# Optimization experiments

Measured on AMD Instinct MI355X. Metric: run time of the kernel, lower is better.

## Reference

```python
import jax, jax.numpy as jnp
import numpy as np

DIM = 768
NUM_HEAD = 12
DIM_HEAD = DIM // NUM_HEAD
SCALE = DIM_HEAD ** -0.5
B, N = 4, 1024


def setup_inputs() -> dict:
    key = jax.random.key(0)
    ks = jax.random.split(key, 6)
    return {
        "x": jax.random.normal(ks[0], (B, N, DIM), jnp.float32),
        "q_weight": jax.random.normal(ks[1], (DIM, DIM), jnp.float32) * 0.02,
        "k_weight": jax.random.normal(ks[2], (DIM, DIM), jnp.float32) * 0.02,
        "v_weight": jax.random.normal(ks[3], (DIM, DIM), jnp.float32) * 0.02,
        "q_bias": jnp.zeros((DIM,), jnp.float32),
        "k_bias": jnp.zeros((DIM,), jnp.float32),
        "v_bias": jnp.zeros((DIM,), jnp.float32),
        "proj_weight": jax.random.normal(ks[4], (DIM, DIM), jnp.float32) * 0.02,
        "proj_bias": jax.random.normal(ks[5], (DIM,), jnp.float32) * 0.02,
    }


def reference(x, q_weight, k_weight, v_weight, q_bias, k_bias, v_bias,
              proj_weight, proj_bias):
    B_, N_, C = x.shape
    shortcut = x
    # pre-norm: torch .std() is unbiased (ddof=1)
    mean = jnp.mean(x, axis=-1, keepdims=True)
    std = jnp.std(x, axis=-1, keepdims=True, ddof=1)
    xn = (x - mean) / std
    # F.linear: x @ W.T + b
    q = xn @ q_weight.T + q_bias
    k = xn @ k_weight.T + k_bias
    v = xn @ v_weight.T + v_bias
    # b n (h d) -> b h n d
    q = q.reshape(B_, N_, NUM_HEAD, DIM_HEAD).transpose(0, 2, 1, 3)
    k = k.reshape(B_, N_, NUM_HEAD, DIM_HEAD).transpose(0, 2, 1, 3)
    v = v.reshape(B_, N_, NUM_HEAD, DIM_HEAD).transpose(0, 2, 1, 3)
    attn = jnp.einsum('bhqd,bhkd->bhqk', q, k * SCALE)
    attn = jax.nn.softmax(attn, axis=-1)
    out = jnp.einsum('bhqk,bhkd->bhqd', attn, v)
    out = out.transpose(0, 2, 1, 3).reshape(B_, N_, C)
    out = out @ proj_weight.T + proj_bias
    return out + shortcut
```

## Files before the change

### kernel.cpp

```cpp
#include <hip/hip_runtime.h>

typedef unsigned short ushort_t;
typedef unsigned int uint_t;
typedef __attribute__((ext_vector_type(8))) unsigned short ushort8;
typedef __attribute__((ext_vector_type(2))) unsigned int uint2v;
typedef __attribute__((ext_vector_type(8))) __bf16 bf16x8;
typedef __attribute__((ext_vector_type(4))) float floatx4;

#define DIM 768
#define NHEAD 12
#define DHEAD 64
#define SEQ 1024
#define BATCH 4
#define TOKENS (BATCH * SEQ)
#define WELEM (DIM * DIM)
#define SCALE_LOG2E 0.18033688011112042f

static __device__ __forceinline__ uint_t fbits(float f) {
  union { float f; uint_t u; } c; c.f = f; return c.u;
}
static __device__ __forceinline__ ushort_t f2bf(float f) {
  return (ushort_t)((fbits(f) + 0x8000u) >> 16);
}
static __device__ __forceinline__ uint_t pack_bf2(float lo, float hi) {
  const uint_t a = fbits(lo) + 0x8000u, b = fbits(hi) + 0x8000u;
#if __has_builtin(__builtin_amdgcn_perm)
  return __builtin_amdgcn_perm(b, a, 0x07060302u);
#else
  return (a >> 16) | (b & 0xFFFF0000u);
#endif
}
static __device__ __forceinline__ float fexp2(float x) {
#if __has_builtin(__builtin_amdgcn_exp2f)
  return __builtin_amdgcn_exp2f(x);
#else
  return exp2f(x);
#endif
}
static __device__ __forceinline__ floatx4 mfma16(ushort8 a, ushort8 b, floatx4 c) {
  return __builtin_amdgcn_mfma_f32_16x16x32_bf16(
      __builtin_bit_cast(bf16x8, a), __builtin_bit_cast(bf16x8, b), c, 0, 0, 0);
}
static __device__ __forceinline__ void gload_lds16(const ushort_t* g,
                                                   ushort_t* l) {
  __builtin_amdgcn_global_load_lds(
      (const __attribute__((address_space(1))) void*)g,
      (__attribute__((address_space(3))) void*)l, 16, 0, 0);
}

__global__ __launch_bounds__(256) void prep_kernel(
    const float* __restrict__ qw, const float* __restrict__ kw,
    const float* __restrict__ vw, const float* __restrict__ pw,
    const float* __restrict__ x, ushort_t* __restrict__ wbf,
    ushort_t* __restrict__ xn) {
  const int bid = blockIdx.x;
  if (bid < 2304) {
    const int mat = bid / 576, inner = bid % 576;
    const float* s = (mat == 0) ? qw : (mat == 1) ? kw : (mat == 2) ? vw : pw;
    ushort_t* d = wbf + (size_t)mat * WELEM;
    const int i = (inner * 256 + threadIdx.x) * 4;
    const float4 f = *(const float4*)&s[i];
    uint2v o;
    o[0] = pack_bf2(f.x, f.y);
    o[1] = pack_bf2(f.z, f.w);
    *(uint2v*)&d[i] = o;
  } else {
    const int wave = threadIdx.x >> 6, lane = threadIdx.x & 63;
    const int row = (bid - 2304) * 4 + wave;
    const float4* xr = (const float4*)(x + (size_t)row * DIM);
    float4 v[3];
    float s = 0.f, s2 = 0.f;
#pragma unroll
    for (int j = 0; j < 3; ++j) {
      v[j] = xr[j * 64 + lane];
      s += v[j].x + v[j].y + v[j].z + v[j].w;
      s2 += v[j].x * v[j].x + v[j].y * v[j].y + v[j].z * v[j].z +
            v[j].w * v[j].w;
    }
#pragma unroll
    for (int off = 1; off < 64; off <<= 1) {
      s += __shfl_xor(s, off);
      s2 += __shfl_xor(s2, off);
    }
    const float mean = s * (1.f / 768.f);
    const float var = (s2 - 768.f * mean * mean) * (1.f / 767.f);
    const float rstd = rsqrtf(var);
    ushort_t* xo = xn + (size_t)row * DIM;
#pragma unroll
    for (int j = 0; j < 3; ++j) {
      uint2v o;
      o[0] = pack_bf2((v[j].x - mean) * rstd, (v[j].y - mean) * rstd);
      o[1] = pack_bf2((v[j].z - mean) * rstd, (v[j].w - mean) * rstd);
      *(uint2v*)&xo[(j * 64 + lane) * 4] = o;
    }
  }
}

#define BK 64
#define NKIT (DIM / BK)
__global__ __launch_bounds__(256) void qkv_kernel(
    const ushort_t* __restrict__ xn, const ushort_t* __restrict__ wbf,
    const float* __restrict__ qb, const float* __restrict__ kb,
    const float* __restrict__ vb,
    ushort_t* __restrict__ qh, ushort_t* __restrict__ kh,
    ushort_t* __restrict__ vt) {
  __shared__ ushort_t As[2][128 * BK];
  __shared__ ushort_t Bs[2][128 * BK];
  const int tid = threadIdx.x;
  const int wave = tid >> 6, lane = tid & 63, quad = lane >> 4, l15 = lane & 15;
  const int m0 = blockIdx.x * 128;
  const int mat = blockIdx.y / 6, nb = blockIdx.y % 6;
  const int n0 = nb * 128;
  const ushort_t* W = wbf + (size_t)mat * WELEM;
  const int chan_off = (wave >> 1) * 64, tok_off = (wave & 1) * 64;
  const int srow8 = lane >> 3;
  const int schunk = (lane & 7) ^ srow8;
  const int l7 = l15 & 7;

  floatx4 acc[4][4];
#pragma unroll
  for (int i = 0; i < 4; ++i)
#pragma unroll
    for (int j = 0; j < 4; ++j) acc[i][j] = (floatx4){0.f, 0.f, 0.f, 0.f};

  auto stage = [&](int k0, int bf) {
#pragma unroll
    for (int i = 0; i < 4; ++i) {
      const int c = wave * 4 + i;
      const int row = c * 8 + srow8;
      gload_lds16(&xn[(size_t)(m0 + row) * DIM + k0 + schunk * 8],
                  &As[bf][c * 512]);
      gload_lds16(&W[(size_t)(n0 + row) * DIM + k0 + schunk * 8],
                  &Bs[bf][c * 512]);
    }
  };

  stage(0, 0);
  for (int it = 0; it < NKIT; ++it) {
    const int cur = it & 1;
    __syncthreads();
    if (it + 1 < NKIT) stage((it + 1) * BK, cur ^ 1);
    ushort8 af[4][2], bfr[4][2];
#pragma unroll
    for (int i = 0; i < 4; ++i)
#pragma unroll
      for (int k2 = 0; k2 < 2; ++k2) {
        const int ch = ((k2 * 4 + quad) ^ l7) * 8;
        bfr[i][k2] = *(const ushort8*)&Bs[cur][(chan_off + i * 16 + l15) * BK + ch];
        af[i][k2] = *(const ushort8*)&As[cur][(tok_off + i * 16 + l15) * BK + ch];
      }
#pragma unroll
    for (int k2 = 0; k2 < 2; ++k2)
#pragma unroll
      for (int i = 0; i < 4; ++i)
#pragma unroll
        for (int j = 0; j < 4; ++j)
          acc[i][j] = mfma16(bfr[i][k2], af[j][k2], acc[i][j]);
  }

  if (mat != 2) {
    const float* bias = (mat == 0) ? qb : kb;
    ushort_t* dst = (mat == 0) ? qh : kh;
    const float os = (mat == 0) ? SCALE_LOG2E : 1.0f;
    const int hh = (n0 + chan_off) >> 6;
#pragma unroll
    for (int i = 0; i < 4; ++i) {
      const int ch0 = n0 + chan_off + i * 16 + quad * 4;
      const float4 bv = *(const float4*)&bias[ch0];
      const int d0 = i * 16 + quad * 4;
#pragma unroll
      for (int j = 0; j < 4; ++j) {
        const int tok = m0 + tok_off + j * 16 + l15;
        const int bb = tok >> 10, nn = tok & 1023;
        uint2v pk;
        pk[0] = pack_bf2((acc[i][j][0] + bv.x) * os, (acc[i][j][1] + bv.y) * os);
        pk[1] = pack_bf2((acc[i][j][2] + bv.z) * os, (acc[i][j][3] + bv.w) * os);
        *(uint2v*)&dst[(size_t)((bb * NHEAD + hh) * SEQ + nn) * DHEAD + d0] = pk;
      }
    }
  } else {
    const int tokg = m0 + tok_off;
    const int bb = tokg >> 10, gg = tokg & 1023;
#pragma unroll
    for (int i = 0; i < 4; ++i) {
      const int ch0 = n0 + chan_off + i * 16 + quad * 4;
      const float4 bv = *(const float4*)&vb[ch0];
      const float bvf[4] = {bv.x, bv.y, bv.z, bv.w};
      const int hh = ch0 >> 6, d0 = ch0 & 63;
#pragma unroll
      for (int r = 0; r < 4; ++r) {
        const size_t base = (size_t)((bb * NHEAD + hh) * DHEAD + d0 + r) * SEQ;
        uint2v pk;
        pk[0] = pack_bf2(acc[i][0][r] + bvf[r], acc[i][1][r] + bvf[r]);
        pk[1] = pack_bf2(acc[i][2][r] + bvf[r], acc[i][3][r] + bvf[r]);
        *(uint2v*)&vt[base + gg + l15 * 4] = pk;
      }
    }
  }
}

#define PSTR 68
__global__ __launch_bounds__(256) void attn_kernel(
    const ushort_t* __restrict__ qh, const ushort_t* __restrict__ kh,
    const ushort_t* __restrict__ vt, ushort_t* __restrict__ ao) {
  __shared__ ushort_t kv[2][2][4096];
  __shared__ ushort_t Ps[4][16 * PSTR];
  float* cb = (float*)&kv[0][0][0];
  const int tid = threadIdx.x;
  const int wave = tid >> 6, lane = tid & 63, quad = lane >> 4, l15 = lane & 15;
  const int l7 = l15 & 7;
  const int grp = wave >> 1, wsub = wave & 1;
  const int bid = blockIdx.x;
  const int idx = bid >> 3;
  const int hb = (bid & 7) * 6 + idx % 6;
  const int qb = idx / 6;
  const int h = hb % NHEAD, b = hb / NHEAD;
  const int basekv = ((b * NHEAD + h) * SEQ) * DHEAD;
  const int basevt = ((b * NHEAD + h) * DHEAD) * SEQ;
  const int q0 = qb * 64 + wsub * 32;
  const int kbase = grp * 512;

  ushort8 qf[2][2];
#pragma unroll
  for (int w = 0; w < 2; ++w) {
    const ushort_t* Qr = qh + basekv + (q0 + w * 16 + l15) * DHEAD;
    qf[w][0] = *(const ushort8*)&Qr[quad * 8];
    qf[w][1] = *(const ushort8*)&Qr[32 + quad * 8];
  }
  ushort8 ones;
#pragma unroll
  for (int i = 0; i < 8; ++i) ones[i] = 0x3F80;

  floatx4 o[2][4];
#pragma unroll
  for (int w = 0; w < 2; ++w)
#pragma unroll
    for (int t = 0; t < 4; ++t) o[w][t] = (floatx4){0.f, 0.f, 0.f, 0.f};
  floatx4 acc_l[2] = {(floatx4){0.f, 0.f, 0.f, 0.f},
                      (floatx4){0.f, 0.f, 0.f, 0.f}};

  const int srow8 = lane >> 3, schunk = (lane & 7) ^ srow8;

  for (int kt = 0; kt < 512; kt += 64) {
#pragma unroll
    for (int i = 0; i < 4; ++i) {
      const int c = wsub * 4 + i;
      gload_lds16(&kh[basekv + (kbase + kt + c * 8 + srow8) * DHEAD + schunk * 8],
                  &kv[grp][0][c * 512]);
      gload_lds16(&vt[basevt + (c * 8 + srow8) * SEQ + kbase + kt + schunk * 8],
                  &kv[grp][1][c * 512]);
    }
    __syncthreads();

    floatx4 sacc[2][4];
#pragma unroll
    for (int w = 0; w < 2; ++w)
#pragma unroll
      for (int s = 0; s < 4; ++s) sacc[w][s] = (floatx4){0.f, 0.f, 0.f, 0.f};
#pragma unroll
    for (int s = 0; s < 4; ++s) {
#pragma unroll
      for (int hh = 0; hh < 2; ++hh) {
        const ushort8 kf = *(const ushort8*)&kv[grp][0][(s * 16 + l15) * 64 +
                                                        (((hh * 4 + quad) ^ l7) * 8)];
#pragma unroll
        for (int w = 0; w < 2; ++w)
          sacc[w][s] = mfma16(qf[w][hh], kf, sacc[w][s]);
      }
    }

#pragma unroll
    for (int w = 0; w < 2; ++w) {
#pragma unroll
      for (int r = 0; r < 4; ++r) {
        uint2v pk;
        pk[0] = pack_bf2(fexp2(sacc[w][0][r]), fexp2(sacc[w][1][r]));
        pk[1] = pack_bf2(fexp2(sacc[w][2][r]), fexp2(sacc[w][3][r]));
        *(uint2v*)&Ps[wave][(quad * 4 + r) * PSTR + l15 * 4] = pk;
      }
    }

#pragma unroll
    for (int hh = 0; hh < 2; ++hh) {
      ushort8 pf[2];
#pragma unroll
      for (int w = 0; w < 2; ++w) {
        pf[w] = *(const ushort8*)&Ps[wave][l15 * PSTR + hh * 32 + quad * 8];
        acc_l[w] = mfma16(pf[w], ones, acc_l[w]);
      }
#pragma unroll
      for (int t = 0; t < 4; ++t) {
        const ushort8 vf = *(const ushort8*)&kv[grp][1][(t * 16 + l15) * 64 +
                                                        (((hh * 4 + quad) ^ l7) * 8)];
#pragma unroll
        for (int w = 0; w < 2; ++w) o[w][t] = mfma16(pf[w], vf, o[w][t]);
      }
    }
    __syncthreads();
  }

  const int cb0 = wsub * (32 * 66);
  if (grp == 1) {
#pragma unroll
    for (int w = 0; w < 2; ++w) {
#pragma unroll
      for (int t = 0; t < 4; ++t)
#pragma unroll
        for (int r = 0; r < 4; ++r)
          cb[cb0 + (w * 16 + quad * 4 + r) * 66 + t * 16 + l15] = o[w][t][r];
      if (l15 == 0)
#pragma unroll
        for (int r = 0; r < 4; ++r)
          cb[cb0 + (w * 16 + quad * 4 + r) * 66 + 64] = acc_l[w][r];
    }
  }
  __syncthreads();
  if (grp == 0) {
#pragma unroll
    for (int w = 0; w < 2; ++w) {
#pragma unroll
      for (int r = 0; r < 4; ++r) {
        const int row = w * 16 + quad * 4 + r;
        const float l = acc_l[w][r] + cb[cb0 + row * 66 + 64];
        const float rl = 1.f / l;
        const int token = b * SEQ + q0 + row;
#pragma unroll
        for (int t = 0; t < 4; ++t) {
          const float val = o[w][t][r] + cb[cb0 + row * 66 + t * 16 + l15];
          ao[(size_t)token * DIM + h * DHEAD + t * 16 + l15] = f2bf(val * rl);
        }
      }
    }
  }
}

__global__ __launch_bounds__(256) void proj_kernel(
    const ushort_t* __restrict__ ao, const ushort_t* __restrict__ pwb,
    const float* __restrict__ pb, const float* __restrict__ x,
    float* __restrict__ out) {
  __shared__ ushort_t As[2][64 * BK];
  __shared__ ushort_t Bs[2][128 * BK];
  const int tid = threadIdx.x;
  const int wave = tid >> 6, lane = tid & 63, quad = lane >> 4, l15 = lane & 15;
  const int m0 = blockIdx.x * 64;
  const int n0 = blockIdx.y * 128;
  const int chan_off = (wave >> 1) * 64, tok_off = (wave & 1) * 32;
  const int srow8 = lane >> 3;
  const int schunk = (lane & 7) ^ srow8;
  const int l7 = l15 & 7;

  floatx4 acc[4][2];
#pragma unroll
  for (int i = 0; i < 4; ++i)
#pragma unroll
    for (int j = 0; j < 2; ++j) acc[i][j] = (floatx4){0.f, 0.f, 0.f, 0.f};

  auto stage = [&](int k0, int bf) {
#pragma unroll
    for (int i = 0; i < 2; ++i) {
      const int c = wave * 2 + i;
      const int row = c * 8 + srow8;
      gload_lds16(&ao[(size_t)(m0 + row) * DIM + k0 + schunk * 8],
                  &As[bf][c * 512]);
    }
#pragma unroll
    for (int i = 0; i < 4; ++i) {
      const int c = wave * 4 + i;
      const int row = c * 8 + srow8;
      gload_lds16(&pwb[(size_t)(n0 + row) * DIM + k0 + schunk * 8],
                  &Bs[bf][c * 512]);
    }
  };

  stage(0, 0);
  for (int it = 0; it < NKIT; ++it) {
    const int cur = it & 1;
    __syncthreads();
    if (it + 1 < NKIT) stage((it + 1) * BK, cur ^ 1);
    ushort8 af[2][2], bfr[4][2];
#pragma unroll
    for (int k2 = 0; k2 < 2; ++k2) {
      const int ch = ((k2 * 4 + quad) ^ l7) * 8;
#pragma unroll
      for (int j = 0; j < 2; ++j)
        af[j][k2] = *(const ushort8*)&As[cur][(tok_off + j * 16 + l15) * BK + ch];
#pragma unroll
      for (int i = 0; i < 4; ++i)
        bfr[i][k2] = *(const ushort8*)&Bs[cur][(chan_off + i * 16 + l15) * BK + ch];
    }
#pragma unroll
    for (int k2 = 0; k2 < 2; ++k2)
#pragma unroll
      for (int i = 0; i < 4; ++i)
#pragma unroll
        for (int j = 0; j < 2; ++j)
          acc[i][j] = mfma16(bfr[i][k2], af[j][k2], acc[i][j]);
  }

#pragma unroll
  for (int i = 0; i < 4; ++i) {
    const int ch0 = n0 + chan_off + i * 16 + quad * 4;
    const float4 bv = *(const float4*)&pb[ch0];
#pragma unroll
    for (int j = 0; j < 2; ++j) {
      const int tok = m0 + tok_off + j * 16 + l15;
      const float4 res = *(const float4*)&x[(size_t)tok * DIM + ch0];
      float4 ov;
      ov.x = acc[i][j][0] + bv.x + res.x;
      ov.y = acc[i][j][1] + bv.y + res.y;
      ov.z = acc[i][j][2] + bv.z + res.z;
      ov.w = acc[i][j][3] + bv.w + res.w;
      *(float4*)&out[(size_t)tok * DIM + ch0] = ov;
    }
  }
}

extern "C" void kernel_launch(void* const* d_in, const int* in_sizes, int n_in,
                              void* d_out, int out_size, void* d_ws,
                              size_t ws_size, hipStream_t stream) {
  const float* x  = (const float*)d_in[0];
  const float* qw = (const float*)d_in[1];
  const float* kw = (const float*)d_in[2];
  const float* vw = (const float*)d_in[3];
  const float* qb = (const float*)d_in[4];
  const float* kb = (const float*)d_in[5];
  const float* vb = (const float*)d_in[6];
  const float* pw = (const float*)d_in[7];
  const float* pb = (const float*)d_in[8];
  float* out = (float*)d_out;

  ushort_t* ws = (ushort_t*)d_ws;
  const size_t NTOK = (size_t)TOKENS * DIM;
  ushort_t* xn  = ws;
  ushort_t* qh  = ws + NTOK;
  ushort_t* kh  = ws + 2 * NTOK;
  ushort_t* vt  = ws + 3 * NTOK;
  ushort_t* wbf = ws + 4 * NTOK;
  ushort_t* ao  = xn;

  prep_kernel<<<2304 + TOKENS / 4, 256, 0, stream>>>(qw, kw, vw, pw, x, wbf, xn);
  qkv_kernel<<<dim3(32, 18), 256, 0, stream>>>(xn, wbf, qb, kb, vb, qh, kh, vt);
  attn_kernel<<<768, 256, 0, stream>>>(qh, kh, vt, ao);
  proj_kernel<<<dim3(64, 6), 256, 0, stream>>>(ao, wbf + 3 * (size_t)WELEM, pb,
                                               x, out);
}
```

Before: 152.9 us.

## Halve QKV token tile and double-buffer K/V tiles in attention

The QKV GEMM drops its token tile from 128 to 64 rows per block, which doubles the grid to 1152 blocks for better occupancy and load balance, and the V-transpose epilogue is adjusted to match. The attention kernel switches from single-buffered 64-key tiles with two barriers per iteration to double-buffered 32-key tiles, prefetching the next tile while computing the current one, with one barrier per iteration. The V tile uses a new swizzle for its 32-wide rows, and the probability scratch is split per query sub-tile. The trade-off is less reuse per block in the GEMM and more loop iterations and barriers of smaller MFMA work in attention.

```diff
diff --git a/kernel.cpp b/kernel.cpp
--- a/kernel.cpp
+++ b/kernel.cpp
@@ -104,33 +104,36 @@
     const float* __restrict__ vb,
     ushort_t* __restrict__ qh, ushort_t* __restrict__ kh,
     ushort_t* __restrict__ vt) {
-  __shared__ ushort_t As[2][128 * BK];
+  __shared__ ushort_t As[2][64 * BK];
   __shared__ ushort_t Bs[2][128 * BK];
   const int tid = threadIdx.x;
   const int wave = tid >> 6, lane = tid & 63, quad = lane >> 4, l15 = lane & 15;
-  const int m0 = blockIdx.x * 128;
+  const int m0 = blockIdx.x * 64;
   const int mat = blockIdx.y / 6, nb = blockIdx.y % 6;
   const int n0 = nb * 128;
   const ushort_t* W = wbf + (size_t)mat * WELEM;
-  const int chan_off = (wave >> 1) * 64, tok_off = (wave & 1) * 64;
+  const int chan_off = (wave >> 1) * 64, tok_off = (wave & 1) * 32;
   const int srow8 = lane >> 3;
   const int schunk = (lane & 7) ^ srow8;
   const int l7 = l15 & 7;
 
-  floatx4 acc[4][4];
+  floatx4 acc[4][2];
 #pragma unroll
   for (int i = 0; i < 4; ++i)
 #pragma unroll
-    for (int j = 0; j < 4; ++j) acc[i][j] = (floatx4){0.f, 0.f, 0.f, 0.f};
+    for (int j = 0; j < 2; ++j) acc[i][j] = (floatx4){0.f, 0.f, 0.f, 0.f};
 
   auto stage = [&](int k0, int bf) {
+#pragma unroll
+    for (int i = 0; i < 2; ++i) {
+      const int c = wave * 2 + i;
+      gload_lds16(&xn[(size_t)(m0 + c * 8 + srow8) * DIM + k0 + schunk * 8],
+                  &As[bf][c * 512]);
+    }
 #pragma unroll
     for (int i = 0; i < 4; ++i) {
       const int c = wave * 4 + i;
-      const int row = c * 8 + srow8;
-      gload_lds16(&xn[(size_t)(m0 + row) * DIM + k0 + schunk * 8],
-                  &As[bf][c * 512]);
-      gload_lds16(&W[(size_t)(n0 + row) * DIM + k0 + schunk * 8],
+      gload_lds16(&W[(size_t)(n0 + c * 8 + srow8) * DIM + k0 + schunk * 8],
                   &Bs[bf][c * 512]);
     }
   };
@@ -140,21 +143,23 @@
     const int cur = it & 1;
     __syncthreads();
     if (it + 1 < NKIT) stage((it + 1) * BK, cur ^ 1);
-    ushort8 af[4][2], bfr[4][2];
-#pragma unroll
-    for (int i = 0; i < 4; ++i)
-#pragma unroll
-      for (int k2 = 0; k2 < 2; ++k2) {
-        const int ch = ((k2 * 4 + quad) ^ l7) * 8;
+    ushort8 af[2][2], bfr[4][2];
+#pragma unroll
+    for (int k2 = 0; k2 < 2; ++k2) {
+      const int ch = ((k2 * 4 + quad) ^ l7) * 8;
+#pragma unroll
+      for (int j = 0; j < 2; ++j)
+        af[j][k2] = *(const ushort8*)&As[cur][(tok_off + j * 16 + l15) * BK + ch];
+#pragma unroll
+      for (int i = 0; i < 4; ++i)
         bfr[i][k2] = *(const ushort8*)&Bs[cur][(chan_off + i * 16 + l15) * BK + ch];
-        af[i][k2] = *(const ushort8*)&As[cur][(tok_off + i * 16 + l15) * BK + ch];
-      }
+    }
 #pragma unroll
     for (int k2 = 0; k2 < 2; ++k2)
 #pragma unroll
       for (int i = 0; i < 4; ++i)
 #pragma unroll
-        for (int j = 0; j < 4; ++j)
+        for (int j = 0; j < 2; ++j)
           acc[i][j] = mfma16(bfr[i][k2], af[j][k2], acc[i][j]);
   }
 
@@ -169,7 +174,7 @@
       const float4 bv = *(const float4*)&bias[ch0];
       const int d0 = i * 16 + quad * 4;
 #pragma unroll
-      for (int j = 0; j < 4; ++j) {
+      for (int j = 0; j < 2; ++j) {
         const int tok = m0 + tok_off + j * 16 + l15;
         const int bb = tok >> 10, nn = tok & 1023;
         uint2v pk;
@@ -190,22 +195,20 @@
 #pragma unroll
       for (int r = 0; r < 4; ++r) {
         const size_t base = (size_t)((bb * NHEAD + hh) * DHEAD + d0 + r) * SEQ;
-        uint2v pk;
-        pk[0] = pack_bf2(acc[i][0][r] + bvf[r], acc[i][1][r] + bvf[r]);
-        pk[1] = pack_bf2(acc[i][2][r] + bvf[r], acc[i][3][r] + bvf[r]);
-        *(uint2v*)&vt[base + gg + l15 * 4] = pk;
+        *(uint_t*)&vt[base + gg + l15 * 2] =
+            pack_bf2(acc[i][0][r] + bvf[r], acc[i][1][r] + bvf[r]);
       }
     }
   }
 }
 
-#define PSTR 68
+#define PSTR2 34
 __global__ __launch_bounds__(256) void attn_kernel(
     const ushort_t* __restrict__ qh, const ushort_t* __restrict__ kh,
     const ushort_t* __restrict__ vt, ushort_t* __restrict__ ao) {
-  __shared__ ushort_t kv[2][2][4096];
-  __shared__ ushort_t Ps[4][16 * PSTR];
-  float* cb = (float*)&kv[0][0][0];
+  __shared__ ushort_t kv[2][2][2][2048];
+  __shared__ ushort_t Ps[4][2][16 * PSTR2];
+  float* cb = (float*)&kv[0][0][0][0];
   const int tid = threadIdx.x;
   const int wave = tid >> 6, lane = tid & 63, quad = lane >> 4, l15 = lane & 15;
   const int l7 = l15 & 7;
@@ -239,30 +242,40 @@
   floatx4 acc_l[2] = {(floatx4){0.f, 0.f, 0.f, 0.f},
                       (floatx4){0.f, 0.f, 0.f, 0.f}};
 
-  const int srow8 = lane >> 3, schunk = (lane & 7) ^ srow8;
-
-  for (int kt = 0; kt < 512; kt += 64) {
-#pragma unroll
-    for (int i = 0; i < 4; ++i) {
-      const int c = wsub * 4 + i;
-      gload_lds16(&kh[basekv + (kbase + kt + c * 8 + srow8) * DHEAD + schunk * 8],
-                  &kv[grp][0][c * 512]);
-      gload_lds16(&vt[basevt + (c * 8 + srow8) * SEQ + kbase + kt + schunk * 8],
-                  &kv[grp][1][c * 512]);
-    }
+  const int ksrow = lane >> 3, kschunk = (lane & 7) ^ ksrow;
+  const int vdrow = lane >> 2;
+  const int vchunk = (lane & 3) ^ ((vdrow >> 1) & 3);
+
+  auto stage = [&](int kt, int bf) {
+#pragma unroll
+    for (int i = 0; i < 2; ++i) {
+      const int c = wsub * 2 + i;
+      gload_lds16(&kh[basekv + (kt + c * 8 + ksrow) * DHEAD + kschunk * 8],
+                  &kv[grp][bf][0][c * 512]);
+      gload_lds16(&vt[basevt + (c * 16 + vdrow) * SEQ + kt + vchunk * 8],
+                  &kv[grp][bf][1][c * 512]);
+    }
+  };
+
+  stage(kbase, 0);
+  for (int it = 0; it < 16; ++it) {
+    const int cur = it & 1;
     __syncthreads();
-
-    floatx4 sacc[2][4];
+    if (it + 1 < 16) stage(kbase + (it + 1) * 32, cur ^ 1);
+    const ushort_t* K = &kv[grp][cur][0][0];
+    const ushort_t* V = &kv[grp][cur][1][0];
+
+    floatx4 sacc[2][2];
 #pragma unroll
     for (int w = 0; w < 2; ++w)
 #pragma unroll
-      for (int s = 0; s < 4; ++s) sacc[w][s] = (floatx4){0.f, 0.f, 0.f, 0.f};
-#pragma unroll
-    for (int s = 0; s < 4; ++s) {
+      for (int s = 0; s < 2; ++s) sacc[w][s] = (floatx4){0.f, 0.f, 0.f, 0.f};
+#pragma unroll
+    for (int s = 0; s < 2; ++s) {
 #pragma unroll
       for (int hh = 0; hh < 2; ++hh) {
-        const ushort8 kf = *(const ushort8*)&kv[grp][0][(s * 16 + l15) * 64 +
-                                                        (((hh * 4 + quad) ^ l7) * 8)];
+        const ushort8 kf = *(const ushort8*)&K[(s * 16 + l15) * 64 +
+                                               (((hh * 4 + quad) ^ l7) * 8)];
 #pragma unroll
         for (int w = 0; w < 2; ++w)
           sacc[w][s] = mfma16(qf[w][hh], kf, sacc[w][s]);
@@ -270,34 +283,27 @@
     }
 
 #pragma unroll
+    for (int w = 0; w < 2; ++w)
+#pragma unroll
+      for (int r = 0; r < 4; ++r)
+        *(uint_t*)&Ps[wave][w][(quad * 4 + r) * PSTR2 + l15 * 2] =
+            pack_bf2(fexp2(sacc[w][0][r]), fexp2(sacc[w][1][r]));
+
+    ushort8 pf[2];
+#pragma unroll
     for (int w = 0; w < 2; ++w) {
-#pragma unroll
-      for (int r = 0; r < 4; ++r) {
-        uint2v pk;
-        pk[0] = pack_bf2(fexp2(sacc[w][0][r]), fexp2(sacc[w][1][r]));
-        pk[1] = pack_bf2(fexp2(sacc[w][2][r]), fexp2(sacc[w][3][r]));
-        *(uint2v*)&Ps[wave][(quad * 4 + r) * PSTR + l15 * 4] = pk;
-      }
-    }
-
-#pragma unroll
-    for (int hh = 0; hh < 2; ++hh) {
-      ushort8 pf[2];
-#pragma unroll
-      for (int w = 0; w < 2; ++w) {
-        pf[w] = *(const ushort8*)&Ps[wave][l15 * PSTR + hh * 32 + quad * 8];
-        acc_l[w] = mfma16(pf[w], ones, acc_l[w]);
-      }
-#pragma unroll
-      for (int t = 0; t < 4; ++t) {
-        const ushort8 vf = *(const ushort8*)&kv[grp][1][(t * 16 + l15) * 64 +
-                                                        (((hh * 4 + quad) ^ l7) * 8)];
-#pragma unroll
-        for (int w = 0; w < 2; ++w) o[w][t] = mfma16(pf[w], vf, o[w][t]);
-      }
-    }
-    __syncthreads();
-  }
+      pf[w] = *(const ushort8*)&Ps[wave][w][l15 * PSTR2 + quad * 8];
+      acc_l[w] = mfma16(pf[w], ones, acc_l[w]);
+    }
+#pragma unroll
+    for (int t = 0; t < 4; ++t) {
+      const ushort8 vf = *(const ushort8*)&V[(t * 16 + l15) * 32 +
+                                             ((quad ^ ((l15 >> 1) & 3)) * 8)];
+#pragma unroll
+      for (int w = 0; w < 2; ++w) o[w][t] = mfma16(pf[w], vf, o[w][t]);
+    }
+  }
+  __syncthreads();
 
   const int cb0 = wsub * (32 * 66);
   if (grp == 1) {
@@ -359,15 +365,13 @@
 #pragma unroll
     for (int i = 0; i < 2; ++i) {
       const int c = wave * 2 + i;
-      const int row = c * 8 + srow8;
-      gload_lds16(&ao[(size_t)(m0 + row) * DIM + k0 + schunk * 8],
+      gload_lds16(&ao[(size_t)(m0 + c * 8 + srow8) * DIM + k0 + schunk * 8],
                   &As[bf][c * 512]);
     }
 #pragma unroll
     for (int i = 0; i < 4; ++i) {
       const int c = wave * 4 + i;
-      const int row = c * 8 + srow8;
-      gload_lds16(&pwb[(size_t)(n0 + row) * DIM + k0 + schunk * 8],
+      gload_lds16(&pwb[(size_t)(n0 + c * 8 + srow8) * DIM + k0 + schunk * 8],
                   &Bs[bf][c * 512]);
     }
   };
@@ -439,7 +443,7 @@
   ushort_t* ao  = xn;
 
   prep_kernel<<<2304 + TOKENS / 4, 256, 0, stream>>>(qw, kw, vw, pw, x, wbf, xn);
-  qkv_kernel<<<dim3(32, 18), 256, 0, stream>>>(xn, wbf, qb, kb, vb, qh, kh, vt);
+  qkv_kernel<<<dim3(64, 18), 256, 0, stream>>>(xn, wbf, qb, kb, vb, qh, kh, vt);
   attn_kernel<<<768, 256, 0, stream>>>(qh, kh, vt, ao);
   proj_kernel<<<dim3(64, 6), 256, 0, stream>>>(ao, wbf + 3 * (size_t)WELEM, pb,
                                                x, out);
```

After: 153.6 us. No clear change (+0.5%).
